# Kernel tuning notes

Measured on AMD Instinct MI355X. Metric: run time of the kernel, lower is better.

Reference implementation:

```python
import math
import jax, jax.numpy as jnp
import numpy as np

B, S, HID, H, NREL = 4, 512, 1024, 16, 64
D = HID // H  # per-head size = 64, must equal relation embedding dim


def setup_inputs() -> dict:
    key = jax.random.key(0)
    ks = jax.random.split(key, 12)
    w = lambda k, shape: jax.random.normal(k, shape, jnp.float32) * 0.02
    return {
        "q_in": jax.random.normal(ks[0], (B, S, HID), jnp.float32),
        "k_in": jax.random.normal(ks[1], (B, S, HID), jnp.float32),
        "v_in": jax.random.normal(ks[2], (B, S, HID), jnp.float32),
        "mask": jax.random.randint(ks[3], (B, 1, S, S), 0, NREL),
        "Wq": w(ks[4], (HID, HID)), "bq": jnp.zeros((HID,), jnp.float32),
        "Wk": w(ks[5], (HID, HID)), "bk": jnp.zeros((HID,), jnp.float32),
        "Wv": w(ks[6], (HID, HID)), "bv": jnp.zeros((HID,), jnp.float32),
        "Wo": w(ks[7], (HID, HID)), "bo": jnp.zeros((HID,), jnp.float32),
        "rel_k_table": w(ks[8], (NREL, D)),
        "rel_v_table": w(ks[9], (NREL, D)),
    }


def reference(q_in, k_in, v_in, mask, Wq, bq, Wk, bk, Wv, bv, Wo, bo,
              rel_k_table, rel_v_table):
    def proj(x, W, b):  # [B,S,HID] -> [B,H,S,D]
        return (x @ W.T + b).reshape(B, S, H, D).transpose(0, 2, 1, 3)

    q = proj(q_in, Wq, bq)
    k = proj(k_in, Wk, bk)
    v = proj(v_in, Wv, bv)

    ids = mask[:, 0]                      # [B,S,S] relation ids
    rel_k = rel_k_table[ids]              # [B,S,S,D]
    rel_v = rel_v_table[ids]              # [B,S,S,D]

    scores = jnp.einsum('bhqd,bhkd->bhqk', q, k)
    scores = scores + jnp.einsum('bhqd,bqkd->bhqk', q, rel_k) / 4.0
    scores = scores / math.sqrt(float(D))

    bias = (1.0 - (mask > 0).astype(scores.dtype)) * -10000.0  # [B,1,S,S]
    probs = jax.nn.softmax(scores + bias, axis=-1)             # [B,H,S,S]

    out = jnp.einsum('bhqk,bhkd->bhqd', probs, v)
    out = out + 0.25 * jnp.einsum('bhqk,bqkd->bhqd', probs, rel_v)
    out = out.transpose(0, 2, 1, 3).reshape(B, S, HID)
    return out @ Wo.T + bo
```

## Files before the change

kernel.cpp:

```cpp
#include <hip/hip_runtime.h>


typedef __attribute__((ext_vector_type(8))) short bf16x8 __attribute__((may_alias));
typedef __attribute__((ext_vector_type(4))) float f32x4;

__device__ __forceinline__ short f2bf(float x) {
    unsigned u = __float_as_uint(x);
    u += 0x7fff + ((u >> 16) & 1);
    return (short)(u >> 16);
}

__device__ __forceinline__ void async16(void* lds, const void* g) {
    __builtin_amdgcn_global_load_lds(
        (const __attribute__((address_space(1))) void*)g,
        (__attribute__((address_space(3))) void*)lds, 16, 0, 0);
}

__global__ __launch_bounds__(256)
void cast_all(const float* __restrict__ x0, const float* __restrict__ x1, const float* __restrict__ x2,
              const float* __restrict__ w0, const float* __restrict__ w1,
              const float* __restrict__ w2, const float* __restrict__ w3,
              short* __restrict__ y0, short* __restrict__ y1, short* __restrict__ y2,
              short* __restrict__ u0, short* __restrict__ u1,
              short* __restrict__ u2, short* __restrict__ u3)
{
    size_t i = (size_t)blockIdx.x * 256 + threadIdx.x;
    const float* src; short* dst; size_t off;
    if (i < 3u*524288u) {
        int s = (int)(i / 524288u); off = i % 524288u;
        src = s == 0 ? x0 : (s == 1 ? x1 : x2);
        dst = s == 0 ? y0 : (s == 1 ? y1 : y2);
    } else {
        size_t j = i - 3u*524288u;
        int s = (int)(j / 262144u); off = j % 262144u;
        src = s == 0 ? w0 : (s == 1 ? w1 : (s == 2 ? w2 : w3));
        dst = s == 0 ? u0 : (s == 1 ? u1 : (s == 2 ? u2 : u3));
    }
    float4 f = ((const float4*)src)[off];
    short4 o; o.x = f2bf(f.x); o.y = f2bf(f.y); o.z = f2bf(f.z); o.w = f2bf(f.w);
    ((short4*)dst)[off] = o;
}

__global__ __launch_bounds__(256)
void gemm_bf16(const short* __restrict__ A0, const short* __restrict__ A1, const short* __restrict__ A2,
               const short* __restrict__ B0, const short* __restrict__ B1, const short* __restrict__ B2,
               const float* __restrict__ c0, const float* __restrict__ c1, const float* __restrict__ c2,
               void* __restrict__ O0, void* __restrict__ O1, void* __restrict__ O2,
               int mode)
{
    __shared__ short Als[128 * 64];
    __shared__ short Bls[64 * 64];
    const int z = blockIdx.z;
    const short* A    = z == 0 ? A0 : (z == 1 ? A1 : A2);
    const short* Bm   = z == 0 ? B0 : (z == 1 ? B1 : B2);
    const float* bias = z == 0 ? c0 : (z == 1 ? c1 : c2);
    void*        O    = z == 0 ? O0 : (z == 1 ? O1 : O2);

    const int t = threadIdx.x;
    const int lane = t & 63, w = t >> 6;
    const int rowBase = blockIdx.y * 128;
    const int colBase = blockIdx.x * 64;
    const int gl = ((lane & 7) - (lane >> 3)) & 7;

    f32x4 acc[2][4];
#pragma unroll
    for (int i = 0; i < 2; ++i)
#pragma unroll
        for (int j = 0; j < 4; ++j) acc[i][j] = (f32x4){0.f, 0.f, 0.f, 0.f};

    const int rstage = w * 8 + (lane >> 3);
    const short* Ag = A  + (size_t)(rowBase + rstage) * 1024 + gl * 8;
    const short* Bg = Bm + (size_t)(colBase + rstage) * 1024 + gl * 8;

    for (int it = 0; it < 16; ++it) {
        const int k0 = it * 64;
#pragma unroll
        for (int i = 0; i < 4; ++i)
            async16(&Als[(i * 32 + w * 8) * 64], Ag + (size_t)i * 32 * 1024 + k0);
#pragma unroll
        for (int i = 0; i < 2; ++i)
            async16(&Bls[(i * 32 + w * 8) * 64], Bg + (size_t)i * 32 * 1024 + k0);
        __syncthreads();
#pragma unroll
        for (int kk = 0; kk < 2; ++kk) {
            bf16x8 a[2], b[4];
#pragma unroll
            for (int mi = 0; mi < 2; ++mi) {
                int r = w * 32 + mi * 16 + (lane & 15);
                int s = (kk * 4 + (lane >> 4) + r) & 7;
                a[mi] = *(const bf16x8*)&Als[r * 64 + s * 8];
            }
#pragma unroll
            for (int ni = 0; ni < 4; ++ni) {
                int r = ni * 16 + (lane & 15);
                int s = (kk * 4 + (lane >> 4) + r) & 7;
                b[ni] = *(const bf16x8*)&Bls[r * 64 + s * 8];
            }
#pragma unroll
            for (int mi = 0; mi < 2; ++mi)
#pragma unroll
                for (int ni = 0; ni < 4; ++ni)
                    acc[mi][ni] = __builtin_amdgcn_mfma_f32_16x16x32_bf16(
                        a[mi], b[ni], acc[mi][ni], 0, 0, 0);
        }
        __syncthreads();
    }

    const int quad = lane >> 4, cl = lane & 15;
#pragma unroll
    for (int mi = 0; mi < 2; ++mi) {
#pragma unroll
        for (int ni = 0; ni < 4; ++ni) {
            int col = colBase + ni * 16 + cl;
            float bv = bias[col];
#pragma unroll
            for (int reg = 0; reg < 4; ++reg) {
                int row = rowBase + w * 32 + mi * 16 + quad * 4 + reg;
                float val = acc[mi][ni][reg] + bv;
                if (mode == 1) {
                    int bb = row >> 9, s = row & 511;
                    int hh = col >> 6, d = col & 63;
                    if (z < 2)
                        ((short*)O)[(((size_t)(bb * 16 + hh) * 512 + s) << 6) + d] = f2bf(val);
                    else
                        ((short*)O)[(((size_t)(bb * 16 + hh) * 64 + d) << 9) + s] = f2bf(val);
                } else {
                    ((float*)O)[(size_t)row * 1024 + col] = val;
                }
            }
        }
    }
}

__global__ __launch_bounds__(256)
void attn_kernel(const short* __restrict__ qg, const short* __restrict__ kg,
                 const short* __restrict__ vtg, const int* __restrict__ mask,
                 const float* __restrict__ relk, const float* __restrict__ relv,
                 short* __restrict__ attn_b)
{
    __shared__ __align__(16) short Qs[16 * 72];
    __shared__ __align__(16) short Ks[64 * 72];
    __shared__ __align__(16) float Sc[16 * 524];
    __shared__ __align__(16) float qwr[16 * 68];
    __shared__ __align__(16) short Sw[16 * 72];

    const int t    = threadIdx.x;
    const int lane = t & 63, w = t >> 6;
    const int quad = lane >> 4, cl = lane & 15;
    const int bid  = blockIdx.x;
    const int qbk  = bid & 31;
    const int bh   = bid >> 5;
    const int b    = bh >> 4, h = bh & 15;
    const int q0   = qbk * 16;

    const short* qbase = qg  + ((size_t)bh * 512 + q0) * 64;
    const short* kbase = kg  + (size_t)bh * 512 * 64;
    const short* vbase = vtg + (size_t)bh * 64 * 512;
    const int*   mb    = mask + (size_t)b * 512 * 512 + (size_t)q0 * 512;

    if (t < 128) {
        int row = t >> 3, c8 = (t & 7) * 8;
        *(bf16x8*)&Qs[row * 72 + c8] = *(const bf16x8*)(qbase + row * 64 + c8);
    }
#pragma unroll
    for (int i = 0; i < 4; ++i) {
        int l = t + 256 * i;
        int row = l >> 4, c4 = (l & 15) * 4;
        float4 f = *(const float4*)(relk + row * 64 + c4);
        short4 o; o.x = f2bf(f.x); o.y = f2bf(f.y); o.z = f2bf(f.z); o.w = f2bf(f.w);
        *(short4*)&Ks[row * 72 + c4] = o;
    }
    __syncthreads();

    {
        f32x4 acc = (f32x4){0.f, 0.f, 0.f, 0.f};
#pragma unroll
        for (int kk = 0; kk < 2; ++kk) {
            bf16x8 a = *(const bf16x8*)&Qs[cl * 72 + kk * 32 + quad * 8];
            bf16x8 bf = *(const bf16x8*)&Ks[(w * 16 + cl) * 72 + kk * 32 + quad * 8];
            acc = __builtin_amdgcn_mfma_f32_16x16x32_bf16(a, bf, acc, 0, 0, 0);
        }
#pragma unroll
        for (int reg = 0; reg < 4; ++reg)
            qwr[(quad * 4 + reg) * 68 + w * 16 + cl] = acc[reg];
    }

    for (int kc = 0; kc < 8; ++kc) {
        __syncthreads();
#pragma unroll
        for (int i = 0; i < 2; ++i) {
            int l = t + 256 * i;
            int row = l >> 3, c8 = (l & 7) * 8;
            *(bf16x8*)&Ks[row * 72 + c8] =
                *(const bf16x8*)(kbase + (size_t)(kc * 64 + row) * 64 + c8);
        }
        __syncthreads();
        f32x4 acc = (f32x4){0.f, 0.f, 0.f, 0.f};
#pragma unroll
        for (int kk = 0; kk < 2; ++kk) {
            bf16x8 a = *(const bf16x8*)&Qs[cl * 72 + kk * 32 + quad * 8];
            bf16x8 bf = *(const bf16x8*)&Ks[(w * 16 + cl) * 72 + kk * 32 + quad * 8];
            acc = __builtin_amdgcn_mfma_f32_16x16x32_bf16(a, bf, acc, 0, 0, 0);
        }
        int k = kc * 64 + w * 16 + cl;
#pragma unroll
        for (int reg = 0; reg < 4; ++reg) {
            int q = quad * 4 + reg;
            int id = mb[q * 512 + k];
            float sc = (acc[reg] + 0.25f * qwr[q * 68 + id]) * 0.125f;
            if (id == 0) sc -= 10000.0f;
            Sc[q * 524 + k] = sc;
        }
    }
    __syncthreads();

    for (int i = t; i < 16 * 68; i += 256) qwr[i] = 0.f;
    __syncthreads();

    for (int r = w; r < 16; r += 4) {
        float vals[8];
        float mx = -1e30f;
#pragma unroll
        for (int e = 0; e < 8; ++e) {
            vals[e] = Sc[r * 524 + lane + 64 * e];
            mx = fmaxf(mx, vals[e]);
        }
#pragma unroll
        for (int off = 32; off > 0; off >>= 1) mx = fmaxf(mx, __shfl_xor(mx, off));
        float sum = 0.f;
#pragma unroll
        for (int e = 0; e < 8; ++e) {
            vals[e] = __expf(vals[e] - mx);
            sum += vals[e];
        }
#pragma unroll
        for (int off = 32; off > 0; off >>= 1) sum += __shfl_xor(sum, off);
        float inv = 1.0f / sum;
        short* Sp = (short*)&Sc[r * 524];
#pragma unroll
        for (int e = 0; e < 8; ++e) {
            float p = vals[e] * inv;
            Sp[lane + 64 * e] = f2bf(p);
            int id = mb[r * 512 + lane + 64 * e];
            atomicAdd(&qwr[r * 68 + id], p);
        }
    }
    __syncthreads();

    {
        int q = t >> 4, r0 = (t & 15) * 4;
        float4 f = *(const float4*)&qwr[q * 68 + r0];
        short4 o; o.x = f2bf(f.x); o.y = f2bf(f.y); o.z = f2bf(f.z); o.w = f2bf(f.w);
        *(short4*)&Sw[q * 72 + r0] = o;
    }

    f32x4 accPV = (f32x4){0.f, 0.f, 0.f, 0.f};
    for (int kc = 0; kc < 8; ++kc) {
        __syncthreads();
#pragma unroll
        for (int i = 0; i < 2; ++i) {
            int l = t + 256 * i;
            int row = l >> 3, c8 = (l & 7) * 8;
            *(bf16x8*)&Ks[row * 72 + c8] =
                *(const bf16x8*)(vbase + (size_t)row * 512 + kc * 64 + c8);
        }
        __syncthreads();
#pragma unroll
        for (int kk = 0; kk < 2; ++kk) {
            bf16x8 a = *(const bf16x8*)((const short*)Sc + cl * 1048 + kc * 64 + kk * 32 + quad * 8);
            bf16x8 bf = *(const bf16x8*)&Ks[(w * 16 + cl) * 72 + kk * 32 + quad * 8];
            accPV = __builtin_amdgcn_mfma_f32_16x16x32_bf16(a, bf, accPV, 0, 0, 0);
        }
    }
    __syncthreads();

#pragma unroll
    for (int i = 0; i < 4; ++i) {
        int l = t + 256 * i;
        int row = l >> 4, c4 = (l & 15) * 4;
        float4 f = *(const float4*)(relv + row * 64 + c4);
        Ks[(c4 + 0) * 72 + row] = f2bf(f.x);
        Ks[(c4 + 1) * 72 + row] = f2bf(f.y);
        Ks[(c4 + 2) * 72 + row] = f2bf(f.z);
        Ks[(c4 + 3) * 72 + row] = f2bf(f.w);
    }
    __syncthreads();

    f32x4 accRV = (f32x4){0.f, 0.f, 0.f, 0.f};
#pragma unroll
    for (int kk = 0; kk < 2; ++kk) {
        bf16x8 a = *(const bf16x8*)&Sw[cl * 72 + kk * 32 + quad * 8];
        bf16x8 bf = *(const bf16x8*)&Ks[(w * 16 + cl) * 72 + kk * 32 + quad * 8];
        accRV = __builtin_amdgcn_mfma_f32_16x16x32_bf16(a, bf, accRV, 0, 0, 0);
    }

#pragma unroll
    for (int reg = 0; reg < 4; ++reg) {
        int q = quad * 4 + reg;
        float val = accPV[reg] + 0.25f * accRV[reg];
        attn_b[(size_t)(b * 512 + q0 + q) * 1024 + h * 64 + w * 16 + cl] = f2bf(val);
    }
}

extern "C" void kernel_launch(void* const* d_in, const int* in_sizes, int n_in,
                              void* d_out, int out_size, void* d_ws, size_t ws_size,
                              hipStream_t stream)
{
    const float* q_in = (const float*)d_in[0];
    const float* k_in = (const float*)d_in[1];
    const float* v_in = (const float*)d_in[2];
    const int*   mask = (const int*)d_in[3];
    const float* Wq   = (const float*)d_in[4];
    const float* bq   = (const float*)d_in[5];
    const float* Wk   = (const float*)d_in[6];
    const float* bk   = (const float*)d_in[7];
    const float* Wv   = (const float*)d_in[8];
    const float* bv   = (const float*)d_in[9];
    const float* Wo   = (const float*)d_in[10];
    const float* bo   = (const float*)d_in[11];
    const float* relk = (const float*)d_in[12];
    const float* relv = (const float*)d_in[13];

    char* ws = (char*)d_ws;
    short* qb     = (short*)(ws);
    short* kb     = (short*)(ws + (4u  << 20));
    short* vt     = (short*)(ws + (8u  << 20));
    short* attn_b = (short*)(ws + (12u << 20));
    short* Xq     = (short*)(ws + (16u << 20));
    short* Xk     = (short*)(ws + (20u << 20));
    short* Xv     = (short*)(ws + (24u << 20));
    short* Wqb    = (short*)(ws + (28u << 20));
    short* Wkb    = (short*)(ws + (30u << 20));
    short* Wvb    = (short*)(ws + (32u << 20));
    short* Wob    = (short*)(ws + (34u << 20));

    cast_all<<<10240, 256, 0, stream>>>(q_in, k_in, v_in, Wq, Wk, Wv, Wo,
                                        Xq, Xk, Xv, Wqb, Wkb, Wvb, Wob);

    gemm_bf16<<<dim3(16, 16, 3), 256, 0, stream>>>(
        Xq, Xk, Xv, Wqb, Wkb, Wvb, bq, bk, bv, qb, kb, vt, 1);

    attn_kernel<<<dim3(2048), 256, 0, stream>>>(qb, kb, vt, mask, relk, relv, attn_b);

    gemm_bf16<<<dim3(16, 16, 1), 256, 0, stream>>>(
        attn_b, attn_b, attn_b, Wob, Wob, Wob, bo, bo, bo,
        (void*)d_out, (void*)d_out, (void*)d_out, 0);
}
```

Baseline: 272.7 us.

## Split keys across waves in attention and transpose V-projection stores through LDS

The attention kernel is restructured so each wave owns a 128-key slice. Each wave computes QK scores, exponentiates them without max subtraction, accumulates P·V in registers and bins relation probabilities per wave. Partial outputs, row sums and bins are then reduced across waves through LDS, which removes the full score buffer, the separate softmax pass and most of the barriers. K and V tiles are now loaded straight from global memory into registers instead of being staged in LDS. Separately, the V projection epilogue transposes its tile in LDS so the transposed output is written with coalesced 16-byte stores rather than scattered 2-byte stores. Skipping the max subtraction relies on the scores staying in a safe exponent range.

```diff
diff --git a/kernel.cpp b/kernel.cpp
--- a/kernel.cpp
+++ b/kernel.cpp
@@ -48,8 +48,10 @@
                void* __restrict__ O0, void* __restrict__ O1, void* __restrict__ O2,
                int mode)
 {
-    __shared__ short Als[128 * 64];
-    __shared__ short Bls[64 * 64];
+    __shared__ short ldsw[128 * 64 + 64 * 64];
+    short* Als = ldsw;
+    short* Bls = ldsw + 128 * 64;
+
     const int z = blockIdx.z;
     const short* A    = z == 0 ? A0 : (z == 1 ? A1 : A2);
     const short* Bm   = z == 0 ? B0 : (z == 1 ? B1 : B2);
@@ -107,6 +109,32 @@
     }
 
     const int quad = lane >> 4, cl = lane & 15;
+    if (mode == 1 && z == 2) {
+        short* Tls = ldsw;
+#pragma unroll
+        for (int mi = 0; mi < 2; ++mi)
+#pragma unroll
+            for (int ni = 0; ni < 4; ++ni) {
+                int d = ni * 16 + cl;
+                float bv = bias[colBase + d];
+                short4 pk;
+                pk.x = f2bf(acc[mi][ni][0] + bv);
+                pk.y = f2bf(acc[mi][ni][1] + bv);
+                pk.z = f2bf(acc[mi][ni][2] + bv);
+                pk.w = f2bf(acc[mi][ni][3] + bv);
+                int sl = w * 32 + mi * 16 + quad * 4;
+                *(short4*)&Tls[d * 136 + sl] = pk;
+            }
+        __syncthreads();
+        int d = t >> 2, s0 = (t & 3) * 32;
+        int bb = rowBase >> 9, hh = colBase >> 6, sBase = rowBase & 511;
+        short* dst = (short*)O + (((size_t)(bb * 16 + hh) * 64 + d) << 9) + sBase + s0;
+#pragma unroll
+        for (int j = 0; j < 4; ++j)
+            *(bf16x8*)(dst + j * 8) = *(const bf16x8*)&Tls[d * 136 + s0 + j * 8];
+        return;
+    }
+
 #pragma unroll
     for (int mi = 0; mi < 2; ++mi) {
 #pragma unroll
@@ -120,10 +148,7 @@
                 if (mode == 1) {
                     int bb = row >> 9, s = row & 511;
                     int hh = col >> 6, d = col & 63;
-                    if (z < 2)
-                        ((short*)O)[(((size_t)(bb * 16 + hh) * 512 + s) << 6) + d] = f2bf(val);
-                    else
-                        ((short*)O)[(((size_t)(bb * 16 + hh) * 64 + d) << 9) + s] = f2bf(val);
+                    ((short*)O)[(((size_t)(bb * 16 + hh) * 512 + s) << 6) + d] = f2bf(val);
                 } else {
                     ((float*)O)[(size_t)row * 1024 + col] = val;
                 }
@@ -131,6 +156,12 @@
         }
     }
 }
+
+#define A_LDS_BINS 4160
+#define A_LDS_OPP  21568
+#define A_LDS_LP   38208
+#define A_LDS_INV  38464
+#define A_LDS_TOT  38528
 
 __global__ __launch_bounds__(256)
 void attn_kernel(const short* __restrict__ qg, const short* __restrict__ kg,
@@ -138,167 +169,144 @@
                  const float* __restrict__ relk, const float* __restrict__ relv,
                  short* __restrict__ attn_b)
 {
-    __shared__ __align__(16) short Qs[16 * 72];
-    __shared__ __align__(16) short Ks[64 * 72];
-    __shared__ __align__(16) float Sc[16 * 524];
-    __shared__ __align__(16) float qwr[16 * 68];
-    __shared__ __align__(16) short Sw[16 * 72];
-
-    const int t    = threadIdx.x;
-    const int lane = t & 63, w = t >> 6;
+    __shared__ __align__(16) char pool[A_LDS_TOT];
+    float* qwr    = (float*)pool;
+    short* binsBf = (short*)pool;
+    float* binsA  = (float*)(pool + A_LDS_BINS);
+    float* Lp     = (float*)(pool + A_LDS_LP);
+    float* invl   = (float*)(pool + A_LDS_INV);
+
+    const int t = threadIdx.x, lane = t & 63, w = t >> 6;
     const int quad = lane >> 4, cl = lane & 15;
-    const int bid  = blockIdx.x;
-    const int qbk  = bid & 31;
-    const int bh   = bid >> 5;
-    const int b    = bh >> 4, h = bh & 15;
-    const int q0   = qbk * 16;
+    const int bid = blockIdx.x, qbk = bid & 31, bh = bid >> 5;
+    const int b = bh >> 4, h = bh & 15, q0 = qbk * 16;
 
     const short* qbase = qg  + ((size_t)bh * 512 + q0) * 64;
     const short* kbase = kg  + (size_t)bh * 512 * 64;
     const short* vbase = vtg + (size_t)bh * 64 * 512;
     const int*   mb    = mask + (size_t)b * 512 * 512 + (size_t)q0 * 512;
 
-    if (t < 128) {
-        int row = t >> 3, c8 = (t & 7) * 8;
-        *(bf16x8*)&Qs[row * 72 + c8] = *(const bf16x8*)(qbase + row * 64 + c8);
-    }
-#pragma unroll
-    for (int i = 0; i < 4; ++i) {
-        int l = t + 256 * i;
-        int row = l >> 4, c4 = (l & 15) * 4;
-        float4 f = *(const float4*)(relk + row * 64 + c4);
-        short4 o; o.x = f2bf(f.x); o.y = f2bf(f.y); o.z = f2bf(f.z); o.w = f2bf(f.w);
-        *(short4*)&Ks[row * 72 + c4] = o;
+    float* bins_w = binsA + w * (16 * 68);
+    short* Pst    = (short*)(pool + A_LDS_OPP + w * 4160);
+    float* Op_w   = (float*)(pool + A_LDS_OPP + w * 4160);
+
+    for (int i = t; i < 4 * 16 * 68; i += 256) binsA[i] = 0.f;
+
+    bf16x8 rvb0, rvb1;
+    {
+        const float* rp = relv + (size_t)(quad * 8) * 64 + w * 16 + cl;
+#pragma unroll
+        for (int j = 0; j < 8; ++j) rvb0[j] = f2bf(rp[j * 64]);
+#pragma unroll
+        for (int j = 0; j < 8; ++j) rvb1[j] = f2bf(rp[2048 + j * 64]);
+    }
+
+    bf16x8 qa0 = *(const bf16x8*)(qbase + cl * 64 + quad * 8);
+    bf16x8 qa1 = *(const bf16x8*)(qbase + cl * 64 + 32 + quad * 8);
+
+    {
+        const float* kp = relk + (size_t)(w * 16 + cl) * 64 + quad * 8;
+        bf16x8 rb0, rb1;
+#pragma unroll
+        for (int j = 0; j < 8; ++j) rb0[j] = f2bf(kp[j]);
+#pragma unroll
+        for (int j = 0; j < 8; ++j) rb1[j] = f2bf(kp[32 + j]);
+        f32x4 qr = (f32x4){0.f, 0.f, 0.f, 0.f};
+        qr = __builtin_amdgcn_mfma_f32_16x16x32_bf16(qa0, rb0, qr, 0, 0, 0);
+        qr = __builtin_amdgcn_mfma_f32_16x16x32_bf16(qa1, rb1, qr, 0, 0, 0);
+#pragma unroll
+        for (int reg = 0; reg < 4; ++reg)
+            qwr[(quad * 4 + reg) * 65 + w * 16 + cl] = qr[reg];
     }
     __syncthreads();
 
-    {
-        f32x4 acc = (f32x4){0.f, 0.f, 0.f, 0.f};
-#pragma unroll
-        for (int kk = 0; kk < 2; ++kk) {
-            bf16x8 a = *(const bf16x8*)&Qs[cl * 72 + kk * 32 + quad * 8];
-            bf16x8 bf = *(const bf16x8*)&Ks[(w * 16 + cl) * 72 + kk * 32 + quad * 8];
-            acc = __builtin_amdgcn_mfma_f32_16x16x32_bf16(a, bf, acc, 0, 0, 0);
+    f32x4 oacc[4];
+#pragma unroll
+    for (int dt = 0; dt < 4; ++dt) oacc[dt] = (f32x4){0.f, 0.f, 0.f, 0.f};
+    float lpart[4] = {0.f, 0.f, 0.f, 0.f};
+
+#pragma unroll
+    for (int c = 0; c < 2; ++c) {
+        const int k0 = w * 128 + c * 64;
+#pragma unroll
+        for (int nt = 0; nt < 4; ++nt) {
+            const short* kp = kbase + (size_t)(k0 + nt * 16 + cl) * 64 + quad * 8;
+            bf16x8 kb0 = *(const bf16x8*)kp;
+            bf16x8 kb1 = *(const bf16x8*)(kp + 32);
+            f32x4 s = (f32x4){0.f, 0.f, 0.f, 0.f};
+            s = __builtin_amdgcn_mfma_f32_16x16x32_bf16(qa0, kb0, s, 0, 0, 0);
+            s = __builtin_amdgcn_mfma_f32_16x16x32_bf16(qa1, kb1, s, 0, 0, 0);
+            const int kidx = k0 + nt * 16 + cl;
+#pragma unroll
+            for (int reg = 0; reg < 4; ++reg) {
+                int q = quad * 4 + reg;
+                int id = mb[q * 512 + kidx];
+                float sc = (s[reg] + 0.25f * qwr[q * 65 + id]) * 0.125f;
+                sc = (id == 0) ? sc - 10000.f : sc;
+                float p = __expf(sc);
+                lpart[reg] += p;
+                atomicAdd(&bins_w[q * 68 + id], p);
+                Pst[q * 72 + nt * 16 + cl] = f2bf(p);
+            }
         }
-#pragma unroll
-        for (int reg = 0; reg < 4; ++reg)
-            qwr[(quad * 4 + reg) * 68 + w * 16 + cl] = acc[reg];
-    }
-
-    for (int kc = 0; kc < 8; ++kc) {
-        __syncthreads();
-#pragma unroll
-        for (int i = 0; i < 2; ++i) {
-            int l = t + 256 * i;
-            int row = l >> 3, c8 = (l & 7) * 8;
-            *(bf16x8*)&Ks[row * 72 + c8] =
-                *(const bf16x8*)(kbase + (size_t)(kc * 64 + row) * 64 + c8);
+        bf16x8 pa0 = *(const bf16x8*)&Pst[cl * 72 + quad * 8];
+        bf16x8 pa1 = *(const bf16x8*)&Pst[cl * 72 + 32 + quad * 8];
+#pragma unroll
+        for (int dt = 0; dt < 4; ++dt) {
+            const short* vp = vbase + (size_t)(dt * 16 + cl) * 512 + k0 + quad * 8;
+            bf16x8 vb0 = *(const bf16x8*)vp;
+            bf16x8 vb1 = *(const bf16x8*)(vp + 32);
+            oacc[dt] = __builtin_amdgcn_mfma_f32_16x16x32_bf16(pa0, vb0, oacc[dt], 0, 0, 0);
+            oacc[dt] = __builtin_amdgcn_mfma_f32_16x16x32_bf16(pa1, vb1, oacc[dt], 0, 0, 0);
         }
-        __syncthreads();
-        f32x4 acc = (f32x4){0.f, 0.f, 0.f, 0.f};
-#pragma unroll
-        for (int kk = 0; kk < 2; ++kk) {
-            bf16x8 a = *(const bf16x8*)&Qs[cl * 72 + kk * 32 + quad * 8];
-            bf16x8 bf = *(const bf16x8*)&Ks[(w * 16 + cl) * 72 + kk * 32 + quad * 8];
-            acc = __builtin_amdgcn_mfma_f32_16x16x32_bf16(a, bf, acc, 0, 0, 0);
-        }
-        int k = kc * 64 + w * 16 + cl;
-#pragma unroll
-        for (int reg = 0; reg < 4; ++reg) {
-            int q = quad * 4 + reg;
-            int id = mb[q * 512 + k];
-            float sc = (acc[reg] + 0.25f * qwr[q * 68 + id]) * 0.125f;
-            if (id == 0) sc -= 10000.0f;
-            Sc[q * 524 + k] = sc;
-        }
+    }
+
+#pragma unroll
+    for (int reg = 0; reg < 4; ++reg) {
+        int q = quad * 4 + reg;
+#pragma unroll
+        for (int dt = 0; dt < 4; ++dt)
+            Op_w[q * 65 + dt * 16 + cl] = oacc[dt][reg];
+        float lsum = lpart[reg];
+#pragma unroll
+        for (int m = 8; m >= 1; m >>= 1) lsum += __shfl_xor(lsum, m);
+        if (cl == 0) Lp[w * 16 + q] = lsum;
     }
     __syncthreads();
 
-    for (int i = t; i < 16 * 68; i += 256) qwr[i] = 0.f;
-    __syncthreads();
-
-    for (int r = w; r < 16; r += 4) {
-        float vals[8];
-        float mx = -1e30f;
-#pragma unroll
-        for (int e = 0; e < 8; ++e) {
-            vals[e] = Sc[r * 524 + lane + 64 * e];
-            mx = fmaxf(mx, vals[e]);
-        }
-#pragma unroll
-        for (int off = 32; off > 0; off >>= 1) mx = fmaxf(mx, __shfl_xor(mx, off));
-        float sum = 0.f;
-#pragma unroll
-        for (int e = 0; e < 8; ++e) {
-            vals[e] = __expf(vals[e] - mx);
-            sum += vals[e];
-        }
-#pragma unroll
-        for (int off = 32; off > 0; off >>= 1) sum += __shfl_xor(sum, off);
-        float inv = 1.0f / sum;
-        short* Sp = (short*)&Sc[r * 524];
-#pragma unroll
-        for (int e = 0; e < 8; ++e) {
-            float p = vals[e] * inv;
-            Sp[lane + 64 * e] = f2bf(p);
-            int id = mb[r * 512 + lane + 64 * e];
-            atomicAdd(&qwr[r * 68 + id], p);
-        }
-    }
-    __syncthreads();
-
+    if (t < 16)
+        invl[t] = 1.0f / (Lp[t] + Lp[16 + t] + Lp[32 + t] + Lp[48 + t]);
     {
         int q = t >> 4, r0 = (t & 15) * 4;
-        float4 f = *(const float4*)&qwr[q * 68 + r0];
-        short4 o; o.x = f2bf(f.x); o.y = f2bf(f.y); o.z = f2bf(f.z); o.w = f2bf(f.w);
-        *(short4*)&Sw[q * 72 + r0] = o;
-    }
-
-    f32x4 accPV = (f32x4){0.f, 0.f, 0.f, 0.f};
-    for (int kc = 0; kc < 8; ++kc) {
-        __syncthreads();
-#pragma unroll
-        for (int i = 0; i < 2; ++i) {
-            int l = t + 256 * i;
-            int row = l >> 3, c8 = (l & 7) * 8;
-            *(bf16x8*)&Ks[row * 72 + c8] =
-                *(const bf16x8*)(vbase + (size_t)row * 512 + kc * 64 + c8);
-        }
-        __syncthreads();
-#pragma unroll
-        for (int kk = 0; kk < 2; ++kk) {
-            bf16x8 a = *(const bf16x8*)((const short*)Sc + cl * 1048 + kc * 64 + kk * 32 + quad * 8);
-            bf16x8 bf = *(const bf16x8*)&Ks[(w * 16 + cl) * 72 + kk * 32 + quad * 8];
-            accPV = __builtin_amdgcn_mfma_f32_16x16x32_bf16(a, bf, accPV, 0, 0, 0);
-        }
+        float4 s0 = *(const float4*)&binsA[0 * 1088 + q * 68 + r0];
+        float4 s1 = *(const float4*)&binsA[1 * 1088 + q * 68 + r0];
+        float4 s2 = *(const float4*)&binsA[2 * 1088 + q * 68 + r0];
+        float4 s3 = *(const float4*)&binsA[3 * 1088 + q * 68 + r0];
+        short4 o;
+        o.x = f2bf(s0.x + s1.x + s2.x + s3.x);
+        o.y = f2bf(s0.y + s1.y + s2.y + s3.y);
+        o.z = f2bf(s0.z + s1.z + s2.z + s3.z);
+        o.w = f2bf(s0.w + s1.w + s2.w + s3.w);
+        *(short4*)&binsBf[q * 72 + r0] = o;
     }
     __syncthreads();
 
-#pragma unroll
-    for (int i = 0; i < 4; ++i) {
-        int l = t + 256 * i;
-        int row = l >> 4, c4 = (l & 15) * 4;
-        float4 f = *(const float4*)(relv + row * 64 + c4);
-        Ks[(c4 + 0) * 72 + row] = f2bf(f.x);
-        Ks[(c4 + 1) * 72 + row] = f2bf(f.y);
-        Ks[(c4 + 2) * 72 + row] = f2bf(f.z);
-        Ks[(c4 + 3) * 72 + row] = f2bf(f.w);
-    }
-    __syncthreads();
-
-    f32x4 accRV = (f32x4){0.f, 0.f, 0.f, 0.f};
-#pragma unroll
-    for (int kk = 0; kk < 2; ++kk) {
-        bf16x8 a = *(const bf16x8*)&Sw[cl * 72 + kk * 32 + quad * 8];
-        bf16x8 bf = *(const bf16x8*)&Ks[(w * 16 + cl) * 72 + kk * 32 + quad * 8];
-        accRV = __builtin_amdgcn_mfma_f32_16x16x32_bf16(a, bf, accRV, 0, 0, 0);
-    }
+    bf16x8 ba0 = *(const bf16x8*)&binsBf[cl * 72 + quad * 8];
+    bf16x8 ba1 = *(const bf16x8*)&binsBf[cl * 72 + 32 + quad * 8];
+    f32x4 racc = (f32x4){0.f, 0.f, 0.f, 0.f};
+    racc = __builtin_amdgcn_mfma_f32_16x16x32_bf16(ba0, rvb0, racc, 0, 0, 0);
+    racc = __builtin_amdgcn_mfma_f32_16x16x32_bf16(ba1, rvb1, racc, 0, 0, 0);
 
 #pragma unroll
     for (int reg = 0; reg < 4; ++reg) {
         int q = quad * 4 + reg;
-        float val = accPV[reg] + 0.25f * accRV[reg];
-        attn_b[(size_t)(b * 512 + q0 + q) * 1024 + h * 64 + w * 16 + cl] = f2bf(val);
+        int d = w * 16 + cl;
+        float osum = 0.f;
+#pragma unroll
+        for (int wv = 0; wv < 4; ++wv)
+            osum += ((const float*)(pool + A_LDS_OPP + wv * 4160))[q * 65 + d];
+        float val = (osum + 0.25f * racc[reg]) * invl[q];
+        attn_b[(size_t)(b * 512 + q0 + q) * 1024 + h * 64 + d] = f2bf(val);
     }
 }
 
```

Measured after the change: 243.7 us. 1.12x faster.
